# Optimization experiments

Hardware: AMD Instinct MI355X
Metric: run time of the kernel (lower is better)

The kernel has to match this reference:

```python
import jax, jax.numpy as jnp
import numpy as np

N_NODES = 50000
N_EDGES = 800000
IN_FEATS = 128
N_HIDDEN = 128
N_CLASSES = 41


def setup_inputs() -> dict:
    key = jax.random.key(0)
    ks = jax.random.split(key, 8)
    x = jax.random.normal(ks[0], (N_NODES, IN_FEATS), dtype=jnp.float32)
    src = jax.random.randint(ks[1], (N_EDGES,), 0, N_NODES, dtype=jnp.int32)
    dst = jax.random.randint(ks[2], (N_EDGES,), 0, N_NODES, dtype=jnp.int32)
    # Xavier-ish init for linear weights (stored as [in, out])
    def lin(k, fan_in, fan_out):
        s = (2.0 / (fan_in + fan_out)) ** 0.5
        return jax.random.normal(k, (fan_in, fan_out), dtype=jnp.float32) * s
    return {
        "x": x, "src": src, "dst": dst,
        "W_self0": lin(ks[3], IN_FEATS, N_HIDDEN),
        "W_neigh0": lin(ks[4], IN_FEATS, N_HIDDEN),
        "b0": jnp.zeros((N_HIDDEN,), jnp.float32),
        "W_self1": lin(ks[5], N_HIDDEN, N_CLASSES),
        "W_neigh1": lin(ks[6], N_HIDDEN, N_CLASSES),
        "b1": jnp.zeros((N_CLASSES,), jnp.float32),
    }


def _sage_conv(h, src, dst, W_self, W_neigh, b, n_nodes):
    # mean aggregation over in-neighbors: gather -> segment_sum -> divide by degree
    msg = h[src]  # [E, d]
    agg = jax.ops.segment_sum(msg, dst, num_segments=n_nodes)  # [N, d]
    deg = jax.ops.segment_sum(jnp.ones((src.shape[0],), h.dtype), dst, num_segments=n_nodes)
    agg = agg / jnp.maximum(deg, 1.0)[:, None]  # zero in-degree -> 0 (DGL semantics)
    return h @ W_self + agg @ W_neigh + b


def reference(x, src, dst, W_self0, W_neigh0, b0, W_self1, W_neigh1, b1):
    n = x.shape[0]
    h = _sage_conv(x, src, dst, W_self0, W_neigh0, b0, n)
    h = jax.nn.relu(h)  # dropout is identity in eval mode
    h = _sage_conv(h, src, dst, W_self1, W_neigh1, b1, n)
    return h
```

## Files before the change

kernel.cpp:

```cpp
#include <hip/hip_runtime.h>
#include <hip/hip_bf16.h>

#define N_NODES 50000
#define N_EDGES 800000
#define F 128
#define NC 41
#define SCAN_BLK 256
#define N_SCAN_BLKS ((N_NODES + SCAN_BLK - 1) / SCAN_BLK)
#define NSLICE 8
#define SLICE_NODES (N_NODES / NSLICE)
#define FILL_BLKS_PER_SLICE 256

typedef __attribute__((ext_vector_type(4))) float f32x4;
typedef __attribute__((ext_vector_type(8))) short bf16x8;

__device__ __forceinline__ float bf2f(unsigned short u) {
    unsigned int x = ((unsigned int)u) << 16;
    return __uint_as_float(x);
}
__device__ __forceinline__ unsigned short f2bf(float f) {
    unsigned int x = __float_as_uint(f);
    unsigned int lsb = (x >> 16) & 1u;
    x += 0x7fffu + lsb;
    return (unsigned short)(x >> 16);
}

__global__ __launch_bounds__(256) void count_deg_sliced_kernel(const int* __restrict__ dst,
                                                               int* __restrict__ deg) {
    int slice = blockIdx.x & (NSLICE - 1);
    int bid = blockIdx.x >> 3;
    int lo = slice * SLICE_NODES, hi = lo + SLICE_NODES;
    int stride = FILL_BLKS_PER_SLICE * 256;
    for (int e = bid * 256 + threadIdx.x; e < N_EDGES; e += stride) {
        int d = dst[e];
        if (d >= lo && d < hi) atomicAdd(&deg[d], 1);
    }
}

__global__ __launch_bounds__(SCAN_BLK) void scan1_kernel(const int* __restrict__ deg,
                                                         int* __restrict__ local,
                                                         int* __restrict__ bsum) {
    __shared__ int buf[SCAN_BLK];
    int tid = threadIdx.x;
    int i = blockIdx.x * SCAN_BLK + tid;
    int v = (i < N_NODES) ? deg[i] : 0;
    buf[tid] = v;
    __syncthreads();
#pragma unroll
    for (int off = 1; off < SCAN_BLK; off <<= 1) {
        int t = (tid >= off) ? buf[tid - off] : 0;
        __syncthreads();
        buf[tid] += t;
        __syncthreads();
    }
    if (i < N_NODES) local[i] = buf[tid] - v;
    if (tid == SCAN_BLK - 1) bsum[blockIdx.x] = buf[tid];
}

__global__ __launch_bounds__(SCAN_BLK) void scan2_kernel(int* __restrict__ bsum,
                                                         int* __restrict__ row_ptr) {
    __shared__ int buf[SCAN_BLK];
    int tid = threadIdx.x;
    int v = (tid < N_SCAN_BLKS) ? bsum[tid] : 0;
    buf[tid] = v;
    __syncthreads();
#pragma unroll
    for (int off = 1; off < SCAN_BLK; off <<= 1) {
        int t = (tid >= off) ? buf[tid - off] : 0;
        __syncthreads();
        buf[tid] += t;
        __syncthreads();
    }
    if (tid < N_SCAN_BLKS) bsum[tid] = buf[tid] - v;
    if (tid == SCAN_BLK - 1) row_ptr[N_NODES] = buf[tid];
}

__global__ __launch_bounds__(SCAN_BLK) void scan3_kernel(const int* __restrict__ deg,
                                                         const int* __restrict__ local,
                                                         const int* __restrict__ bsum,
                                                         int* __restrict__ row_ptr,
                                                         int* __restrict__ cursor,
                                                         float* __restrict__ inv_deg) {
    int i = blockIdx.x * SCAN_BLK + threadIdx.x;
    if (i < N_NODES) {
        int rp = local[i] + bsum[blockIdx.x];
        row_ptr[i] = rp;
        cursor[i] = rp;
        inv_deg[i] = 1.0f / fmaxf((float)deg[i], 1.0f);
    }
}

__global__ __launch_bounds__(256) void fill_csr_sliced_kernel(const int* __restrict__ src,
                                                              const int* __restrict__ dst,
                                                              int* __restrict__ cursor,
                                                              int* __restrict__ csr_src) {
    int slice = blockIdx.x & (NSLICE - 1);
    int bid = blockIdx.x >> 3;
    int lo = slice * SLICE_NODES, hi = lo + SLICE_NODES;
    int stride = FILL_BLKS_PER_SLICE * 256;
    for (int e = bid * 256 + threadIdx.x; e < N_EDGES; e += stride) {
        int d = dst[e];
        if (d >= lo && d < hi) {
            int p = atomicAdd(&cursor[d], 1);
            csr_src[p] = src[e];
        }
    }
}

__global__ void pack_w_kernel(const float* __restrict__ Ws0, const float* __restrict__ Wn0,
                              const float* __restrict__ Ws1, const float* __restrict__ Wn1,
                              unsigned short* __restrict__ Bpk0,
                              unsigned short* __restrict__ Bpk1) {
    int i = blockIdx.x * blockDim.x + threadIdx.x;
    if (i < 128 * 256) {
        int j = i & 7, l = (i >> 3) & 63, kb = (i >> 9) & 3, ct = i >> 11;
        int k = kb * 32 + (l >> 4) * 8 + j;
        int c = ct * 16 + (l & 15);
        float v = (c < F) ? Ws0[k * F + c] : Wn0[k * F + (c - F)];
        Bpk0[i] = f2bf(v);
    } else if (i < 128 * 256 + 128 * 128) {
        int i2 = i - 128 * 256;
        int j = i2 & 7, l = (i2 >> 3) & 63, kb = (i2 >> 9) & 3, ct = i2 >> 11;
        int k = kb * 32 + (l >> 4) * 8 + j;
        int c = ct * 16 + (l & 15);
        float v = 0.0f;
        if (c < 48) { if (c < NC) v = Ws1[k * NC + c]; }
        else if (c >= 64 && c < 112) { int cc = c - 64; if (cc < NC) v = Wn1[k * NC + cc]; }
        Bpk1[i2] = f2bf(v);
    }
}

template<bool AF32, int CT, int MODE>
__global__ __launch_bounds__(256) void gemm_mfma_kernel(const void* __restrict__ Av,
                                                        const unsigned short* __restrict__ Bpk,
                                                        int M,
                                                        unsigned short* __restrict__ outA,
                                                        unsigned short* __restrict__ outB) {
    __shared__ unsigned short As[64 * 128];
    int tid = threadIdx.x;
    int wave = tid >> 6, lane = tid & 63;
    int row0 = blockIdx.x * 64;

    if (AF32) {
        const float* A = (const float*)Av;
#pragma unroll
        for (int i = 0; i < 8; ++i) {
            int fid = tid + i * 256;
            int row = fid >> 5, c4 = (fid & 31) * 4;
            int grow = row0 + row; if (grow > M - 1) grow = M - 1;
            f32x4 v = *(const f32x4*)(A + (size_t)grow * F + c4);
            unsigned int p0 = (unsigned)f2bf(v.x) | ((unsigned)f2bf(v.y) << 16);
            unsigned int p1 = (unsigned)f2bf(v.z) | ((unsigned)f2bf(v.w) << 16);
            int idx = (row * 128 + c4) ^ ((row & 7) << 3);
            *(uint2*)&As[idx] = make_uint2(p0, p1);
        }
    } else {
        const unsigned short* A = (const unsigned short*)Av;
#pragma unroll
        for (int i = 0; i < 4; ++i) {
            int fid = tid + i * 256;
            int row = fid >> 4, c8 = (fid & 15) * 8;
            int grow = row0 + row; if (grow > M - 1) grow = M - 1;
            uint4 v = *(const uint4*)&A[(size_t)grow * F + c8];
            int idx = (row * 128 + c8) ^ ((row & 7) << 3);
            *(uint4*)&As[idx] = v;
        }
    }
    __syncthreads();

    f32x4 acc[4][CT];
#pragma unroll
    for (int m = 0; m < 4; ++m)
#pragma unroll
        for (int n = 0; n < CT; ++n) acc[m][n] = (f32x4){0.f, 0.f, 0.f, 0.f};

#pragma unroll
    for (int kb = 0; kb < 4; ++kb) {
        bf16x8 afr[4];
#pragma unroll
        for (int m = 0; m < 4; ++m) {
            int row = m * 16 + (lane & 15);
            int ke = kb * 32 + (lane >> 4) * 8;
            int idx = (row * 128 + ke) ^ ((row & 7) << 3);
            afr[m] = *(const bf16x8*)&As[idx];
        }
#pragma unroll
        for (int n = 0; n < CT; ++n) {
            int ct = wave * CT + n;
            bf16x8 bfr = *(const bf16x8*)&Bpk[((ct * 4 + kb) * 64 + lane) * 8];
#pragma unroll
            for (int m = 0; m < 4; ++m)
                acc[m][n] = __builtin_amdgcn_mfma_f32_16x16x32_bf16(afr[m], bfr, acc[m][n], 0, 0, 0);
        }
    }

#pragma unroll
    for (int m = 0; m < 4; ++m) {
#pragma unroll
        for (int i = 0; i < 4; ++i) {
            int r = row0 + m * 16 + (lane >> 4) * 4 + i;
            if (r < M) {
#pragma unroll
                for (int n = 0; n < CT; ++n) {
                    int c = (wave * CT + n) * 16 + (lane & 15);
                    unsigned short val = f2bf(acc[m][n][i]);
                    if (MODE == 0) {
                        outA[(size_t)r * (CT * 64) + c] = val;
                    } else {
                        if (c < 48) outA[(size_t)r * 48 + c] = val;
                        else if (c >= 64 && c < 112) outB[(size_t)r * 48 + (c - 64)] = val;
                    }
                }
            }
        }
    }
}

__global__ __launch_bounds__(256) void agg0_kernel(const unsigned int* __restrict__ u,
                                                   const int* __restrict__ row_ptr,
                                                   const int* __restrict__ csr_src,
                                                   const float* __restrict__ inv_deg,
                                                   const float* __restrict__ b0,
                                                   unsigned int* __restrict__ hu) {
    int node = blockIdx.x * 4 + (threadIdx.x >> 6);
    int t = threadIdx.x & 63;
    int s = row_ptr[node], e = row_ptr[node + 1];
    float ax = 0.f, ay = 0.f, bx = 0.f, by = 0.f;
    int j = s;
    for (; j + 7 < e; j += 8) {
        int sr0 = csr_src[j],     sr1 = csr_src[j + 1];
        int sr2 = csr_src[j + 2], sr3 = csr_src[j + 3];
        int sr4 = csr_src[j + 4], sr5 = csr_src[j + 5];
        int sr6 = csr_src[j + 6], sr7 = csr_src[j + 7];
        unsigned int v0 = u[(size_t)sr0 * 128 + 64 + t];
        unsigned int v1 = u[(size_t)sr1 * 128 + 64 + t];
        unsigned int v2 = u[(size_t)sr2 * 128 + 64 + t];
        unsigned int v3 = u[(size_t)sr3 * 128 + 64 + t];
        unsigned int v4 = u[(size_t)sr4 * 128 + 64 + t];
        unsigned int v5 = u[(size_t)sr5 * 128 + 64 + t];
        unsigned int v6 = u[(size_t)sr6 * 128 + 64 + t];
        unsigned int v7 = u[(size_t)sr7 * 128 + 64 + t];
        ax += bf2f((unsigned short)(v0 & 0xffffu)) + bf2f((unsigned short)(v1 & 0xffffu));
        ay += bf2f((unsigned short)(v0 >> 16)) + bf2f((unsigned short)(v1 >> 16));
        bx += bf2f((unsigned short)(v2 & 0xffffu)) + bf2f((unsigned short)(v3 & 0xffffu));
        by += bf2f((unsigned short)(v2 >> 16)) + bf2f((unsigned short)(v3 >> 16));
        ax += bf2f((unsigned short)(v4 & 0xffffu)) + bf2f((unsigned short)(v5 & 0xffffu));
        ay += bf2f((unsigned short)(v4 >> 16)) + bf2f((unsigned short)(v5 >> 16));
        bx += bf2f((unsigned short)(v6 & 0xffffu)) + bf2f((unsigned short)(v7 & 0xffffu));
        by += bf2f((unsigned short)(v6 >> 16)) + bf2f((unsigned short)(v7 >> 16));
    }
    for (; j < e; ++j) {
        int sr = csr_src[j];
        unsigned int v = u[(size_t)sr * 128 + 64 + t];
        ax += bf2f((unsigned short)(v & 0xffffu));
        ay += bf2f((unsigned short)(v >> 16));
    }
    ax += bx; ay += by;
    float inv = inv_deg[node];
    unsigned int vs = u[(size_t)node * 128 + t];
    float2 bb = ((const float2*)b0)[t];
    float h0 = fmaxf(bf2f((unsigned short)(vs & 0xffffu)) + ax * inv + bb.x, 0.0f);
    float h1 = fmaxf(bf2f((unsigned short)(vs >> 16)) + ay * inv + bb.y, 0.0f);
    hu[(size_t)node * 64 + t] = (unsigned)f2bf(h0) | ((unsigned)f2bf(h1) << 16);
}

__global__ __launch_bounds__(256) void final_out_kernel(const unsigned int* __restrict__ ts,
                                                        const unsigned int* __restrict__ tn,
                                                        const int* __restrict__ row_ptr,
                                                        const int* __restrict__ csr_src,
                                                        const float* __restrict__ inv_deg,
                                                        const float* __restrict__ b1,
                                                        float* __restrict__ out) {
    int node = blockIdx.x * 4 + (threadIdx.x >> 6);
    int lane = threadIdx.x & 63;
    int group = lane >> 5;
    int c = lane & 31;
    int s = row_ptr[node], e = row_ptr[node + 1];
    float ax = 0.f, ay = 0.f, bx = 0.f, by = 0.f;
    int j = s + group;
    for (; j + 14 < e; j += 16) {
        int sr0 = csr_src[j],      sr1 = csr_src[j + 2];
        int sr2 = csr_src[j + 4],  sr3 = csr_src[j + 6];
        int sr4 = csr_src[j + 8],  sr5 = csr_src[j + 10];
        int sr6 = csr_src[j + 12], sr7 = csr_src[j + 14];
        unsigned int v0 = tn[(size_t)sr0 * 24 + c];
        unsigned int v1 = tn[(size_t)sr1 * 24 + c];
        unsigned int v2 = tn[(size_t)sr2 * 24 + c];
        unsigned int v3 = tn[(size_t)sr3 * 24 + c];
        unsigned int v4 = tn[(size_t)sr4 * 24 + c];
        unsigned int v5 = tn[(size_t)sr5 * 24 + c];
        unsigned int v6 = tn[(size_t)sr6 * 24 + c];
        unsigned int v7 = tn[(size_t)sr7 * 24 + c];
        ax += bf2f((unsigned short)(v0 & 0xffffu)) + bf2f((unsigned short)(v1 & 0xffffu));
        ay += bf2f((unsigned short)(v0 >> 16)) + bf2f((unsigned short)(v1 >> 16));
        bx += bf2f((unsigned short)(v2 & 0xffffu)) + bf2f((unsigned short)(v3 & 0xffffu));
        by += bf2f((unsigned short)(v2 >> 16)) + bf2f((unsigned short)(v3 >> 16));
        ax += bf2f((unsigned short)(v4 & 0xffffu)) + bf2f((unsigned short)(v5 & 0xffffu));
        ay += bf2f((unsigned short)(v4 >> 16)) + bf2f((unsigned short)(v5 >> 16));
        bx += bf2f((unsigned short)(v6 & 0xffffu)) + bf2f((unsigned short)(v7 & 0xffffu));
        by += bf2f((unsigned short)(v6 >> 16)) + bf2f((unsigned short)(v7 >> 16));
    }
    for (; j < e; j += 2) {
        int sr = csr_src[j];
        unsigned int v = tn[(size_t)sr * 24 + c];
        ax += bf2f((unsigned short)(v & 0xffffu));
        ay += bf2f((unsigned short)(v >> 16));
    }
    ax += bx; ay += by;
    ax += __shfl(ax, lane + 32, 64);
    ay += __shfl(ay, lane + 32, 64);
    if (lane >= 24) return;
    float inv = inv_deg[node];
    unsigned int vs = ts[(size_t)node * 24 + c];
    int c0 = 2 * c, c1 = 2 * c + 1;
    if (c0 < NC)
        out[(size_t)node * NC + c0] = bf2f((unsigned short)(vs & 0xffffu)) + b1[c0] + ax * inv;
    if (c1 < NC)
        out[(size_t)node * NC + c1] = bf2f((unsigned short)(vs >> 16)) + b1[c1] + ay * inv;
}

extern "C" void kernel_launch(void* const* d_in, const int* in_sizes, int n_in,
                              void* d_out, int out_size, void* d_ws, size_t ws_size,
                              hipStream_t stream) {
    const float* x   = (const float*)d_in[0];
    const int*   src = (const int*)d_in[1];
    const int*   dst = (const int*)d_in[2];
    const float* Ws0 = (const float*)d_in[3];
    const float* Wn0 = (const float*)d_in[4];
    const float* b0  = (const float*)d_in[5];
    const float* Ws1 = (const float*)d_in[6];
    const float* Wn1 = (const float*)d_in[7];
    const float* b1  = (const float*)d_in[8];
    float* out = (float*)d_out;

    char* ws = (char*)d_ws;
    size_t o = 0;
    auto alloc = [&](size_t bytes) {
        size_t r = o;
        o = (o + bytes + 255) & ~(size_t)255;
        return r;
    };
    int*   deg     = (int*)(ws + alloc(sizeof(int) * N_NODES));
    int*   local   = (int*)(ws + alloc(sizeof(int) * N_NODES));
    int*   bsum    = (int*)(ws + alloc(sizeof(int) * N_SCAN_BLKS));
    int*   row_ptr = (int*)(ws + alloc(sizeof(int) * (N_NODES + 1)));
    int*   cursor  = (int*)(ws + alloc(sizeof(int) * N_NODES));
    int*   csr     = (int*)(ws + alloc(sizeof(int) * N_EDGES));
    float* inv_deg = (float*)(ws + alloc(sizeof(float) * N_NODES));
    unsigned short* Bpk0 = (unsigned short*)(ws + alloc(sizeof(short) * 128 * 256));
    unsigned short* Bpk1 = (unsigned short*)(ws + alloc(sizeof(short) * 128 * 128));
    unsigned short* u    = (unsigned short*)(ws + alloc(sizeof(short) * (size_t)N_NODES * 256));
    unsigned short* h    = (unsigned short*)(ws + alloc(sizeof(short) * (size_t)N_NODES * 128));
    unsigned short* t_self  = (unsigned short*)(ws + alloc(sizeof(short) * (size_t)N_NODES * 48));
    unsigned short* t_neigh = (unsigned short*)(ws + alloc(sizeof(short) * ((size_t)N_NODES * 48 + 128)));

    hipMemsetAsync(deg, 0, sizeof(int) * N_NODES, stream);
    count_deg_sliced_kernel<<<NSLICE * FILL_BLKS_PER_SLICE, 256, 0, stream>>>(dst, deg);
    scan1_kernel<<<N_SCAN_BLKS, SCAN_BLK, 0, stream>>>(deg, local, bsum);
    scan2_kernel<<<1, SCAN_BLK, 0, stream>>>(bsum, row_ptr);
    scan3_kernel<<<N_SCAN_BLKS, SCAN_BLK, 0, stream>>>(deg, local, bsum, row_ptr, cursor, inv_deg);
    fill_csr_sliced_kernel<<<NSLICE * FILL_BLKS_PER_SLICE, 256, 0, stream>>>(src, dst, cursor, csr);
    pack_w_kernel<<<(128 * 256 + 128 * 128 + 255) / 256, 256, 0, stream>>>(Ws0, Wn0, Ws1, Wn1,
                                                                           Bpk0, Bpk1);

    int nblk = (N_NODES + 63) / 64;
    gemm_mfma_kernel<true, 4, 0><<<nblk, 256, 0, stream>>>(x, Bpk0, N_NODES, u, nullptr);
    agg0_kernel<<<N_NODES / 4, 256, 0, stream>>>((const unsigned int*)u, row_ptr, csr, inv_deg, b0,
                                                 (unsigned int*)h);
    gemm_mfma_kernel<false, 2, 1><<<nblk, 256, 0, stream>>>(h, Bpk1, N_NODES, t_self, t_neigh);
    final_out_kernel<<<N_NODES / 4, 256, 0, stream>>>((const unsigned int*)t_self,
                                                      (const unsigned int*)t_neigh,
                                                      row_ptr, csr, inv_deg, b1, out);
}
```

Baseline: 263.4 us.

## Store neighbor projection in fp8 and fuse CSR build with first GEMM

The first-layer neighbor projection is now written as e4m3-style fp8 instead of bf16, halving the bytes gathered per edge in the first aggregation. The degree count is fused with the weight packing kernel and no longer sliced, and the CSR fill is merged with the first GEMM into one launch so they can run concurrently. This reduces memory traffic and launch count at the cost of extra rounding error in the aggregated features.

Result: no change. 262.1 us (-0.5%).

```diff
diff --git a/kernel.cpp b/kernel.cpp
--- a/kernel.cpp
+++ b/kernel.cpp
@@ -10,6 +10,10 @@
 #define NSLICE 8
 #define SLICE_NODES (N_NODES / NSLICE)
 #define FILL_BLKS_PER_SLICE 256
+#define FILL_BLKS (NSLICE * FILL_BLKS_PER_SLICE)
+#define COUNT_BLKS ((N_EDGES + 255) / 256)
+#define PACK_BLKS ((128 * 256 + 128 * 128) / 256)
+#define GEMM_BLKS ((N_NODES + 63) / 64)
 
 typedef __attribute__((ext_vector_type(4))) float f32x4;
 typedef __attribute__((ext_vector_type(8))) short bf16x8;
@@ -24,16 +28,52 @@
     x += 0x7fffu + lsb;
     return (unsigned short)(x >> 16);
 }
-
-__global__ __launch_bounds__(256) void count_deg_sliced_kernel(const int* __restrict__ dst,
-                                                               int* __restrict__ deg) {
-    int slice = blockIdx.x & (NSLICE - 1);
-    int bid = blockIdx.x >> 3;
-    int lo = slice * SLICE_NODES, hi = lo + SLICE_NODES;
-    int stride = FILL_BLKS_PER_SLICE * 256;
-    for (int e = bid * 256 + threadIdx.x; e < N_EDGES; e += stride) {
-        int d = dst[e];
-        if (d >= lo && d < hi) atomicAdd(&deg[d], 1);
+__device__ __forceinline__ float fp8dec(unsigned int b) {
+    unsigned int t = ((b & 0x80u) << 24) | ((b & 0x7fu) << 20);
+    return __uint_as_float(t) * 0x1.0p+120f;
+}
+__device__ __forceinline__ unsigned char fp8enc(float v) {
+    unsigned int u = __float_as_uint(v);
+    unsigned int s = (u >> 24) & 0x80u;
+    float a = fabsf(v);
+    if (a < 0.015625f) return (unsigned char)s;
+    a = fminf(a, 448.0f);
+    unsigned int b = __float_as_uint(a);
+    b += 0x0007FFFFu + ((b >> 20) & 1u);
+    unsigned int E = (b >> 23) - 120u;
+    unsigned int M = (b >> 20) & 7u;
+    return (unsigned char)(s | (E << 3) | M);
+}
+
+__global__ __launch_bounds__(256) void count_pack_kernel(const int* __restrict__ dst,
+                                                         int* __restrict__ deg,
+                                                         const float* __restrict__ Ws0,
+                                                         const float* __restrict__ Wn0,
+                                                         const float* __restrict__ Ws1,
+                                                         const float* __restrict__ Wn1,
+                                                         unsigned short* __restrict__ Bpk0,
+                                                         unsigned short* __restrict__ Bpk1) {
+    if (blockIdx.x < COUNT_BLKS) {
+        int e = blockIdx.x * 256 + threadIdx.x;
+        if (e < N_EDGES) atomicAdd(&deg[dst[e]], 1);
+    } else {
+        int i = (blockIdx.x - COUNT_BLKS) * 256 + threadIdx.x;
+        if (i < 128 * 256) {
+            int j = i & 7, l = (i >> 3) & 63, kb = (i >> 9) & 3, ct = i >> 11;
+            int k = kb * 32 + (l >> 4) * 8 + j;
+            int c = ct * 16 + (l & 15);
+            float v = (c < F) ? Ws0[k * F + c] : Wn0[k * F + (c - F)];
+            Bpk0[i] = f2bf(v);
+        } else if (i < 128 * 256 + 128 * 128) {
+            int i2 = i - 128 * 256;
+            int j = i2 & 7, l = (i2 >> 3) & 63, kb = (i2 >> 9) & 3, ct = i2 >> 11;
+            int k = kb * 32 + (l >> 4) * 8 + j;
+            int c = ct * 16 + (l & 15);
+            float v = 0.0f;
+            if (c < 48) { if (c < NC) v = Ws1[k * NC + c]; }
+            else if (c >= 64 && c < 112) { int cc = c - 64; if (cc < NC) v = Wn1[k * NC + cc]; }
+            Bpk1[i2] = f2bf(v);
+        }
     }
 }
 
@@ -90,89 +130,51 @@
     }
 }
 
-__global__ __launch_bounds__(256) void fill_csr_sliced_kernel(const int* __restrict__ src,
-                                                              const int* __restrict__ dst,
-                                                              int* __restrict__ cursor,
-                                                              int* __restrict__ csr_src) {
-    int slice = blockIdx.x & (NSLICE - 1);
-    int bid = blockIdx.x >> 3;
-    int lo = slice * SLICE_NODES, hi = lo + SLICE_NODES;
-    int stride = FILL_BLKS_PER_SLICE * 256;
-    for (int e = bid * 256 + threadIdx.x; e < N_EDGES; e += stride) {
-        int d = dst[e];
-        if (d >= lo && d < hi) {
-            int p = atomicAdd(&cursor[d], 1);
-            csr_src[p] = src[e];
-        }
-    }
-}
-
-__global__ void pack_w_kernel(const float* __restrict__ Ws0, const float* __restrict__ Wn0,
-                              const float* __restrict__ Ws1, const float* __restrict__ Wn1,
-                              unsigned short* __restrict__ Bpk0,
-                              unsigned short* __restrict__ Bpk1) {
-    int i = blockIdx.x * blockDim.x + threadIdx.x;
-    if (i < 128 * 256) {
-        int j = i & 7, l = (i >> 3) & 63, kb = (i >> 9) & 3, ct = i >> 11;
-        int k = kb * 32 + (l >> 4) * 8 + j;
-        int c = ct * 16 + (l & 15);
-        float v = (c < F) ? Ws0[k * F + c] : Wn0[k * F + (c - F)];
-        Bpk0[i] = f2bf(v);
-    } else if (i < 128 * 256 + 128 * 128) {
-        int i2 = i - 128 * 256;
-        int j = i2 & 7, l = (i2 >> 3) & 63, kb = (i2 >> 9) & 3, ct = i2 >> 11;
-        int k = kb * 32 + (l >> 4) * 8 + j;
-        int c = ct * 16 + (l & 15);
-        float v = 0.0f;
-        if (c < 48) { if (c < NC) v = Ws1[k * NC + c]; }
-        else if (c >= 64 && c < 112) { int cc = c - 64; if (cc < NC) v = Wn1[k * NC + cc]; }
-        Bpk1[i2] = f2bf(v);
-    }
-}
-
-template<bool AF32, int CT, int MODE>
-__global__ __launch_bounds__(256) void gemm_mfma_kernel(const void* __restrict__ Av,
-                                                        const unsigned short* __restrict__ Bpk,
-                                                        int M,
-                                                        unsigned short* __restrict__ outA,
-                                                        unsigned short* __restrict__ outB) {
+__global__ __launch_bounds__(256) void fill_gemmA_kernel(const int* __restrict__ src,
+                                                         const int* __restrict__ dst,
+                                                         int* __restrict__ cursor,
+                                                         int* __restrict__ csr_src,
+                                                         const float* __restrict__ x,
+                                                         const unsigned short* __restrict__ Bpk,
+                                                         unsigned short* __restrict__ u_self,
+                                                         unsigned char* __restrict__ u_neigh8) {
     __shared__ unsigned short As[64 * 128];
+    if (blockIdx.x < FILL_BLKS) {
+        int slice = blockIdx.x & (NSLICE - 1);
+        int bid = blockIdx.x >> 3;
+        int lo = slice * SLICE_NODES, hi = lo + SLICE_NODES;
+        int stride = FILL_BLKS_PER_SLICE * 256;
+        for (int e = bid * 256 + threadIdx.x; e < N_EDGES; e += stride) {
+            int d = dst[e];
+            if (d >= lo && d < hi) {
+                int p = atomicAdd(&cursor[d], 1);
+                csr_src[p] = src[e];
+            }
+        }
+        return;
+    }
     int tid = threadIdx.x;
     int wave = tid >> 6, lane = tid & 63;
-    int row0 = blockIdx.x * 64;
-
-    if (AF32) {
-        const float* A = (const float*)Av;
-#pragma unroll
-        for (int i = 0; i < 8; ++i) {
-            int fid = tid + i * 256;
-            int row = fid >> 5, c4 = (fid & 31) * 4;
-            int grow = row0 + row; if (grow > M - 1) grow = M - 1;
-            f32x4 v = *(const f32x4*)(A + (size_t)grow * F + c4);
-            unsigned int p0 = (unsigned)f2bf(v.x) | ((unsigned)f2bf(v.y) << 16);
-            unsigned int p1 = (unsigned)f2bf(v.z) | ((unsigned)f2bf(v.w) << 16);
-            int idx = (row * 128 + c4) ^ ((row & 7) << 3);
-            *(uint2*)&As[idx] = make_uint2(p0, p1);
-        }
-    } else {
-        const unsigned short* A = (const unsigned short*)Av;
-#pragma unroll
-        for (int i = 0; i < 4; ++i) {
-            int fid = tid + i * 256;
-            int row = fid >> 4, c8 = (fid & 15) * 8;
-            int grow = row0 + row; if (grow > M - 1) grow = M - 1;
-            uint4 v = *(const uint4*)&A[(size_t)grow * F + c8];
-            int idx = (row * 128 + c8) ^ ((row & 7) << 3);
-            *(uint4*)&As[idx] = v;
-        }
+    int row0 = (blockIdx.x - FILL_BLKS) * 64;
+
+#pragma unroll
+    for (int i = 0; i < 8; ++i) {
+        int fid = tid + i * 256;
+        int row = fid >> 5, c4 = (fid & 31) * 4;
+        int grow = row0 + row; if (grow > N_NODES - 1) grow = N_NODES - 1;
+        f32x4 v = *(const f32x4*)(x + (size_t)grow * F + c4);
+        unsigned int p0 = (unsigned)f2bf(v.x) | ((unsigned)f2bf(v.y) << 16);
+        unsigned int p1 = (unsigned)f2bf(v.z) | ((unsigned)f2bf(v.w) << 16);
+        int idx = (row * 128 + c4) ^ ((row & 7) << 3);
+        *(uint2*)&As[idx] = make_uint2(p0, p1);
     }
     __syncthreads();
 
-    f32x4 acc[4][CT];
+    f32x4 acc[4][4];
 #pragma unroll
     for (int m = 0; m < 4; ++m)
 #pragma unroll
-        for (int n = 0; n < CT; ++n) acc[m][n] = (f32x4){0.f, 0.f, 0.f, 0.f};
+        for (int n = 0; n < 4; ++n) acc[m][n] = (f32x4){0.f, 0.f, 0.f, 0.f};
 
 #pragma unroll
     for (int kb = 0; kb < 4; ++kb) {
@@ -185,8 +187,8 @@
             afr[m] = *(const bf16x8*)&As[idx];
         }
 #pragma unroll
-        for (int n = 0; n < CT; ++n) {
-            int ct = wave * CT + n;
+        for (int n = 0; n < 4; ++n) {
+            int ct = wave * 4 + n;
             bf16x8 bfr = *(const bf16x8*)&Bpk[((ct * 4 + kb) * 64 + lane) * 8];
 #pragma unroll
             for (int m = 0; m < 4; ++m)
@@ -199,24 +201,85 @@
 #pragma unroll
         for (int i = 0; i < 4; ++i) {
             int r = row0 + m * 16 + (lane >> 4) * 4 + i;
-            if (r < M) {
-#pragma unroll
-                for (int n = 0; n < CT; ++n) {
-                    int c = (wave * CT + n) * 16 + (lane & 15);
-                    unsigned short val = f2bf(acc[m][n][i]);
-                    if (MODE == 0) {
-                        outA[(size_t)r * (CT * 64) + c] = val;
-                    } else {
-                        if (c < 48) outA[(size_t)r * 48 + c] = val;
-                        else if (c >= 64 && c < 112) outB[(size_t)r * 48 + (c - 64)] = val;
-                    }
+            if (r < N_NODES) {
+#pragma unroll
+                for (int n = 0; n < 4; ++n) {
+                    int c = (wave * 4 + n) * 16 + (lane & 15);
+                    float v = acc[m][n][i];
+                    if (c < 128) u_self[(size_t)r * 128 + c] = f2bf(v);
+                    else         u_neigh8[(size_t)r * 128 + (c - 128)] = fp8enc(v);
                 }
             }
         }
     }
 }
 
-__global__ __launch_bounds__(256) void agg0_kernel(const unsigned int* __restrict__ u,
+__global__ __launch_bounds__(256) void gemmB_kernel(const unsigned short* __restrict__ A,
+                                                    const unsigned short* __restrict__ Bpk,
+                                                    unsigned short* __restrict__ outA,
+                                                    unsigned short* __restrict__ outB) {
+    __shared__ unsigned short As[64 * 128];
+    int tid = threadIdx.x;
+    int wave = tid >> 6, lane = tid & 63;
+    int row0 = blockIdx.x * 64;
+
+#pragma unroll
+    for (int i = 0; i < 4; ++i) {
+        int fid = tid + i * 256;
+        int row = fid >> 4, c8 = (fid & 15) * 8;
+        int grow = row0 + row; if (grow > N_NODES - 1) grow = N_NODES - 1;
+        uint4 v = *(const uint4*)&A[(size_t)grow * F + c8];
+        int idx = (row * 128 + c8) ^ ((row & 7) << 3);
+        *(uint4*)&As[idx] = v;
+    }
+    __syncthreads();
+
+    f32x4 acc[4][2];
+#pragma unroll
+    for (int m = 0; m < 4; ++m)
+#pragma unroll
+        for (int n = 0; n < 2; ++n) acc[m][n] = (f32x4){0.f, 0.f, 0.f, 0.f};
+
+#pragma unroll
+    for (int kb = 0; kb < 4; ++kb) {
+        bf16x8 afr[4];
+#pragma unroll
+        for (int m = 0; m < 4; ++m) {
+            int row = m * 16 + (lane & 15);
+            int ke = kb * 32 + (lane >> 4) * 8;
+            int idx = (row * 128 + ke) ^ ((row & 7) << 3);
+            afr[m] = *(const bf16x8*)&As[idx];
+        }
+#pragma unroll
+        for (int n = 0; n < 2; ++n) {
+            int ct = wave * 2 + n;
+            bf16x8 bfr = *(const bf16x8*)&Bpk[((ct * 4 + kb) * 64 + lane) * 8];
+#pragma unroll
+            for (int m = 0; m < 4; ++m)
+                acc[m][n] = __builtin_amdgcn_mfma_f32_16x16x32_bf16(afr[m], bfr, acc[m][n], 0, 0, 0);
+        }
+    }
+
+#pragma unroll
+    for (int m = 0; m < 4; ++m) {
+#pragma unroll
+        for (int i = 0; i < 4; ++i) {
+            int r = row0 + m * 16 + (lane >> 4) * 4 + i;
+            if (r < N_NODES) {
+#pragma unroll
+                for (int n = 0; n < 2; ++n) {
+                    int c = (wave * 2 + n) * 16 + (lane & 15);
+                    unsigned short val = f2bf(acc[m][n][i]);
+                    if (c < 48) outA[(size_t)r * 48 + c] = val;
+                    else if (c >= 64 && c < 112) outB[(size_t)r * 48 + (c - 64)] = val;
+                }
+            }
+        }
+    }
+}
+
+__global__ __launch_bounds__(256) void agg0_kernel(const unsigned int* __restrict__ us,
+                                                   const unsigned short* __restrict__ un8,
                                                    const int* __restrict__ row_ptr,
                                                    const int* __restrict__ csr_src,
                                                    const float* __restrict__ inv_deg,
@@ -232,32 +295,32 @@
         int sr2 = csr_src[j + 2], sr3 = csr_src[j + 3];
         int sr4 = csr_src[j + 4], sr5 = csr_src[j + 5];
         int sr6 = csr_src[j + 6], sr7 = csr_src[j + 7];
-        unsigned int v0 = u[(size_t)sr0 * 128 + 64 + t];
-        unsigned int v1 = u[(size_t)sr1 * 128 + 64 + t];
-        unsigned int v2 = u[(size_t)sr2 * 128 + 64 + t];
-        unsigned int v3 = u[(size_t)sr3 * 128 + 64 + t];
-        unsigned int v4 = u[(size_t)sr4 * 128 + 64 + t];
-        unsigned int v5 = u[(size_t)sr5 * 128 + 64 + t];
-        unsigned int v6 = u[(size_t)sr6 * 128 + 64 + t];
-        unsigned int v7 = u[(size_t)sr7 * 128 + 64 + t];
-        ax += bf2f((unsigned short)(v0 & 0xffffu)) + bf2f((unsigned short)(v1 & 0xffffu));
-        ay += bf2f((unsigned short)(v0 >> 16)) + bf2f((unsigned short)(v1 >> 16));
-        bx += bf2f((unsigned short)(v2 & 0xffffu)) + bf2f((unsigned short)(v3 & 0xffffu));
-        by += bf2f((unsigned short)(v2 >> 16)) + bf2f((unsigned short)(v3 >> 16));
-        ax += bf2f((unsigned short)(v4 & 0xffffu)) + bf2f((unsigned short)(v5 & 0xffffu));
-        ay += bf2f((unsigned short)(v4 >> 16)) + bf2f((unsigned short)(v5 >> 16));
-        bx += bf2f((unsigned short)(v6 & 0xffffu)) + bf2f((unsigned short)(v7 & 0xffffu));
-        by += bf2f((unsigned short)(v6 >> 16)) + bf2f((unsigned short)(v7 >> 16));
+        unsigned int w0 = un8[(size_t)sr0 * 64 + t];
+        unsigned int w1 = un8[(size_t)sr1 * 64 + t];
+        unsigned int w2 = un8[(size_t)sr2 * 64 + t];
+        unsigned int w3 = un8[(size_t)sr3 * 64 + t];
+        unsigned int w4 = un8[(size_t)sr4 * 64 + t];
+        unsigned int w5 = un8[(size_t)sr5 * 64 + t];
+        unsigned int w6 = un8[(size_t)sr6 * 64 + t];
+        unsigned int w7 = un8[(size_t)sr7 * 64 + t];
+        ax += fp8dec(w0 & 0xffu) + fp8dec(w1 & 0xffu);
+        ay += fp8dec(w0 >> 8)    + fp8dec(w1 >> 8);
+        bx += fp8dec(w2 & 0xffu) + fp8dec(w3 & 0xffu);
+        by += fp8dec(w2 >> 8)    + fp8dec(w3 >> 8);
+        ax += fp8dec(w4 & 0xffu) + fp8dec(w5 & 0xffu);
+        ay += fp8dec(w4 >> 8)    + fp8dec(w5 >> 8);
+        bx += fp8dec(w6 & 0xffu) + fp8dec(w7 & 0xffu);
+        by += fp8dec(w6 >> 8)    + fp8dec(w7 >> 8);
     }
     for (; j < e; ++j) {
         int sr = csr_src[j];
-        unsigned int v = u[(size_t)sr * 128 + 64 + t];
-        ax += bf2f((unsigned short)(v & 0xffffu));
-        ay += bf2f((unsigned short)(v >> 16));
+        unsigned int w = un8[(size_t)sr * 64 + t];
+        ax += fp8dec(w & 0xffu);
+        ay += fp8dec(w >> 8);
     }
     ax += bx; ay += by;
     float inv = inv_deg[node];
-    unsigned int vs = u[(size_t)node * 128 + t];
+    unsigned int vs = us[(size_t)node * 64 + t];
     float2 bb = ((const float2*)b0)[t];
     float h0 = fmaxf(bf2f((unsigned short)(vs & 0xffffu)) + ax * inv + bb.x, 0.0f);
     float h1 = fmaxf(bf2f((unsigned short)(vs >> 16)) + ay * inv + bb.y, 0.0f);
@@ -349,25 +412,24 @@
     float* inv_deg = (float*)(ws + alloc(sizeof(float) * N_NODES));
     unsigned short* Bpk0 = (unsigned short*)(ws + alloc(sizeof(short) * 128 * 256));
     unsigned short* Bpk1 = (unsigned short*)(ws + alloc(sizeof(short) * 128 * 128));
-    unsigned short* u    = (unsigned short*)(ws + alloc(sizeof(short) * (size_t)N_NODES * 256));
+    unsigned short* u_self = (unsigned short*)(ws + alloc(sizeof(short) * (size_t)N_NODES * 128));
+    unsigned char*  u_nb8  = (unsigned char*)(ws + alloc((size_t)N_NODES * 128));
     unsigned short* h    = (unsigned short*)(ws + alloc(sizeof(short) * (size_t)N_NODES * 128));
     unsigned short* t_self  = (unsigned short*)(ws + alloc(sizeof(short) * (size_t)N_NODES * 48));
     unsigned short* t_neigh = (unsigned short*)(ws + alloc(sizeof(short) * ((size_t)N_NODES * 48 + 128)));
 
     hipMemsetAsync(deg, 0, sizeof(int) * N_NODES, stream);
-    count_deg_sliced_kernel<<<NSLICE * FILL_BLKS_PER_SLICE, 256, 0, stream>>>(dst, deg);
+    count_pack_kernel<<<COUNT_BLKS + PACK_BLKS, 256, 0, stream>>>(dst, deg, Ws0, Wn0, Ws1, Wn1,
+                                                                  Bpk0, Bpk1);
     scan1_kernel<<<N_SCAN_BLKS, SCAN_BLK, 0, stream>>>(deg, local, bsum);
     scan2_kernel<<<1, SCAN_BLK, 0, stream>>>(bsum, row_ptr);
     scan3_kernel<<<N_SCAN_BLKS, SCAN_BLK, 0, stream>>>(deg, local, bsum, row_ptr, cursor, inv_deg);
-    fill_csr_sliced_kernel<<<NSLICE * FILL_BLKS_PER_SLICE, 256, 0, stream>>>(src, dst, cursor, csr);
-    pack_w_kernel<<<(128 * 256 + 128 * 128 + 255) / 256, 256, 0, stream>>>(Ws0, Wn0, Ws1, Wn1,
-                                                                           Bpk0, Bpk1);
-
-    int nblk = (N_NODES + 63) / 64;
-    gemm_mfma_kernel<true, 4, 0><<<nblk, 256, 0, stream>>>(x, Bpk0, N_NODES, u, nullptr);
-    agg0_kernel<<<N_NODES / 4, 256, 0, stream>>>((const unsigned int*)u, row_ptr, csr, inv_deg, b0,
-                                                 (unsigned int*)h);
-    gemm_mfma_kernel<false, 2, 1><<<nblk, 256, 0, stream>>>(h, Bpk1, N_NODES, t_self, t_neigh);
+    fill_gemmA_kernel<<<FILL_BLKS + GEMM_BLKS, 256, 0, stream>>>(src, dst, cursor, csr,
+                                                                 x, Bpk0, u_self, u_nb8);
+    agg0_kernel<<<N_NODES / 4, 256, 0, stream>>>((const unsigned int*)u_self,
+                                                 (const unsigned short*)u_nb8,
+                                                 row_ptr, csr, inv_deg, b0, (unsigned int*)h);
+    gemmB_kernel<<<GEMM_BLKS, 256, 0, stream>>>(h, Bpk1, t_self, t_neigh);
     final_out_kernel<<<N_NODES / 4, 256, 0, stream>>>((const unsigned int*)t_self,
                                                       (const unsigned int*)t_neigh,
                                                       row_ptr, csr, inv_deg, b1, out);
```
